# Kernel tuning notes

Hardware: AMD Instinct MI355X
Metric: run time of the kernel (lower is better)

## Reference

```python
import jax, jax.numpy as jnp
import numpy as np

N = 10000      # nodes
E = 320000     # edges
D = 256        # input_nf = output_nf
H = 256        # hidden_nf
ED = 16        # edges_in_d
NORM = 32.0    # normalization_factor


def setup_inputs() -> dict:
    key = jax.random.key(0)
    ks = jax.random.split(key, 16)
    s = 0.02  # param scale
    return {
        "h": jax.random.normal(ks[0], (N, D), dtype=jnp.float32),
        "edge_index": jax.random.randint(ks[1], (2, E), 0, N, dtype=jnp.int64),
        "edge_attr": jax.random.normal(ks[2], (E, ED), dtype=jnp.float32),
        "node_mask": jnp.ones((N, 1), dtype=jnp.float32),
        "edge_mask": jnp.ones((E, 1), dtype=jnp.float32),
        # edge_mlp: Linear(2D+ED -> H), SiLU, Linear(H -> H), SiLU
        "We1": jax.random.normal(ks[3], (2 * D + ED, H), dtype=jnp.float32) * s,
        "be1": jnp.zeros((H,), dtype=jnp.float32),
        "We2": jax.random.normal(ks[4], (H, H), dtype=jnp.float32) * s,
        "be2": jnp.zeros((H,), dtype=jnp.float32),
        # att_mlp: Linear(H -> 1), Sigmoid
        "Wa": jax.random.normal(ks[5], (H, 1), dtype=jnp.float32) * s,
        "ba": jnp.zeros((1,), dtype=jnp.float32),
        # node_mlp: Linear(H + D -> H), SiLU, Linear(H -> D)
        "Wn1": jax.random.normal(ks[6], (H + D, H), dtype=jnp.float32) * s,
        "bn1": jnp.zeros((H,), dtype=jnp.float32),
        "Wn2": jax.random.normal(ks[7], (H, D), dtype=jnp.float32) * s,
        "bn2": jnp.zeros((D,), dtype=jnp.float32),
    }


def reference(h, edge_index, edge_attr, node_mask, edge_mask,
              We1, be1, We2, be2, Wa, ba, Wn1, bn1, Wn2, bn2):
    row, col = edge_index[0], edge_index[1]
    # edge model: gather endpoints, concat with edge_attr -> [E, 2D+ED]
    e_in = jnp.concatenate([h[row], h[col], edge_attr], axis=1)
    mij = jax.nn.silu(jax.nn.silu(e_in @ We1 + be1) @ We2 + be2)  # [E, H]
    att = jax.nn.sigmoid(mij @ Wa + ba)                            # [E, 1]
    edge_feat = mij * att * edge_mask                              # [E, H]
    # node model: scatter-add messages to rows, normalize by constant
    agg = jax.ops.segment_sum(edge_feat, row, num_segments=h.shape[0]) / NORM  # [N, H]
    a = jnp.concatenate([h, agg], axis=1)                          # [N, D+H]
    h_out = h + (jax.nn.silu(a @ Wn1 + bn1) @ Wn2 + bn2)           # residual
    h_out = h_out * node_mask
    return (h_out, mij)
```

## Files before the change

kernel.cpp:

```cpp
#include <hip/hip_runtime.h>

#define NN 10000
#define NE 320000

typedef __bf16 bf16x8 __attribute__((ext_vector_type(8)));
typedef short  s16x8  __attribute__((ext_vector_type(8)));
typedef float  f32x4  __attribute__((ext_vector_type(4)));

__device__ __forceinline__ unsigned short f2bf(float f) {
  return __builtin_bit_cast(unsigned short, (__bf16)f);
}
__device__ __forceinline__ float bf2f(unsigned short s) {
  unsigned u = ((unsigned)s) << 16;
  return __builtin_bit_cast(float, u);
}
__device__ __forceinline__ float sigm(float x) {
  return __builtin_amdgcn_rcpf(1.0f + __expf(-x));
}
__device__ __forceinline__ float silu_f(float x) {
  return x * __builtin_amdgcn_rcpf(1.0f + __expf(-x));
}

__global__ void prep_w(const float* __restrict__ We1, const float* __restrict__ We2,
                       const float* __restrict__ Wn1, const float* __restrict__ Wn2,
                       unsigned short* __restrict__ W1abT, unsigned short* __restrict__ W1cT,
                       unsigned short* __restrict__ We2T,
                       unsigned short* __restrict__ Wn1T, unsigned short* __restrict__ Wn2T) {
  int g = blockIdx.x * blockDim.x + threadIdx.x;
  const int S1 = 512 * 256, S2 = 256 * 32, S3 = 256 * 256, S4 = 256 * 512, S5 = 256 * 256;
  if (g < S1) {
    int n = g >> 8, k = g & 255;
    float v = (n < 256) ? We1[k * 256 + n] : We1[(256 + k) * 256 + (n - 256)];
    W1abT[g] = f2bf(v);
  } else if (g < S1 + S2) {
    int i = g - S1; int n = i >> 5, kk = i & 31;
    float v = (kk < 16) ? We1[(512 + kk) * 256 + n] : 0.0f;
    W1cT[i] = f2bf(v);
  } else if (g < S1 + S2 + S3) {
    int i = g - S1 - S2; int n = i >> 8, k = i & 255;
    We2T[i] = f2bf(We2[k * 256 + n]);
  } else if (g < S1 + S2 + S3 + S4) {
    int i = g - S1 - S2 - S3; int n = i >> 9, k = i & 511;
    Wn1T[i] = f2bf(Wn1[k * 256 + n]);
  } else if (g < S1 + S2 + S3 + S4 + S5) {
    int i = g - S1 - S2 - S3 - S4; int n = i >> 8, k = i & 255;
    Wn2T[i] = f2bf(Wn2[k * 256 + n]);
  }
}

__global__ void prep_x(const float* __restrict__ h, unsigned short* __restrict__ hb) {
  int g = blockIdx.x * blockDim.x + threadIdx.x;
  if (g < NN * 64) {
    float4 f = ((const float4*)h)[g];
    unsigned short* d = hb + g * 4;
    d[0] = f2bf(f.x); d[1] = f2bf(f.y); d[2] = f2bf(f.z); d[3] = f2bf(f.w);
  }
}

__global__ void hist_kernel(const int* __restrict__ eidx, int* __restrict__ rowi,
                            int* __restrict__ counts) {
  __shared__ int s64;
  if (threadIdx.x == 0) {
    bool b = true;
    for (int i = 1; i < 64; i += 2) b = b && (eidx[i] == 0);
    s64 = b ? 1 : 0;
  }
  __syncthreads();
  int e = blockIdx.x * 256 + threadIdx.x;
  if (e < NE) {
    int r = s64 ? (int)((const long long*)eidx)[e] : eidx[e];
    rowi[e] = r;
    atomicAdd(&counts[r], 1);
  }
}

__global__ __launch_bounds__(1024) void scan_kernel(const int* __restrict__ counts,
                                                    int* __restrict__ rowStart,
                                                    int* __restrict__ cursor) {
  __shared__ int part[1024];
  int t = threadIdx.x;
  int local[10];
  int s = 0;
  #pragma unroll
  for (int i = 0; i < 10; i++) {
    int idx = t * 10 + i;
    int c = (idx < NN) ? counts[idx] : 0;
    local[i] = s; s += c;
  }
  part[t] = s;
  __syncthreads();
  int val = s;
  for (int off = 1; off < 1024; off <<= 1) {
    int tmp = (t >= off) ? part[t - off] : 0;
    __syncthreads();
    part[t] += tmp;
    __syncthreads();
  }
  int base = part[t] - val;
  #pragma unroll
  for (int i = 0; i < 10; i++) {
    int idx = t * 10 + i;
    if (idx < NN) { int v = base + local[i]; rowStart[idx] = v; cursor[idx] = v; }
  }
  if (t == 1023) rowStart[NN] = NE;
}

__global__ void scatter_kernel(const int* __restrict__ rowi, int* __restrict__ cursor,
                               int* __restrict__ eorder, int* __restrict__ rowSorted) {
  int e = blockIdx.x * 256 + threadIdx.x;
  if (e < NE) {
    int r = rowi[e];
    int pos = atomicAdd(&cursor[r], 1);
    eorder[pos] = e;
    rowSorted[pos] = r;
  }
}

__global__ __launch_bounds__(512, 4) void hpq_kernel(
    const unsigned short* __restrict__ hb, const unsigned short* __restrict__ W1abT,
    unsigned short* __restrict__ hPQb) {
  __shared__ unsigned short Abuf[128 * 40];

  const int tid = threadIdx.x;
  const int lane = tid & 63;
  const int wid = tid >> 6;
  const int wrr = wid >> 2, wcc = wid & 3;
  const int n0 = blockIdx.x * 128;
  const int coh = blockIdx.y;
  const unsigned short* Bsrc = W1abT + ((size_t)(coh << 8)) * 256;

  f32x4 acc[4][4];
  #pragma unroll
  for (int m = 0; m < 4; m++)
    #pragma unroll
    for (int n = 0; n < 4; n++) acc[m][n] = (f32x4){0.f, 0.f, 0.f, 0.f};

  const int eA = tid >> 2, sA = tid & 3;
  int nodeA = n0 + eA; if (nodeA >= NN) nodeA = NN - 1;
  const int rbase = (wrr << 6) + (lane & 15);
  const int koff = (lane >> 4) << 3;
  const int cfrag = lane & 15;

  for (int kt = 0; kt < 8; ++kt) {
    const int k0 = kt << 5;
    __syncthreads();
    *(s16x8*)&Abuf[eA * 40 + (sA << 3)] = *(const s16x8*)(hb + (size_t)nodeA * 256 + k0 + (sA << 3));
    __syncthreads();
    bf16x8 a[4], b[4];
    #pragma unroll
    for (int m = 0; m < 4; m++)
      a[m] = __builtin_bit_cast(bf16x8, *(const s16x8*)&Abuf[(rbase + m * 16) * 40 + koff]);
    #pragma unroll
    for (int n = 0; n < 4; n++)
      b[n] = __builtin_bit_cast(bf16x8,
               *(const s16x8*)(Bsrc + (((wcc << 6) + n * 16 + cfrag) << 8) + k0 + koff));
    #pragma unroll
    for (int m = 0; m < 4; m++)
      #pragma unroll
      for (int n = 0; n < 4; n++)
        acc[m][n] = __builtin_amdgcn_mfma_f32_16x16x32_bf16(a[m], b[n], acc[m][n], 0, 0, 0);
  }

  #pragma unroll
  for (int m = 0; m < 4; m++) {
    int rl = (wrr << 6) + m * 16 + ((lane >> 4) << 2);
    #pragma unroll
    for (int n = 0; n < 4; n++) {
      int cg = (wcc << 6) + n * 16 + cfrag;
      #pragma unroll
      for (int j = 0; j < 4; j++) {
        int rg = n0 + rl + j;
        if (rg < NN) hPQb[(size_t)rg * 512 + (coh << 8) + cg] = f2bf(acc[m][n][j]);
      }
    }
  }
}

__global__ __launch_bounds__(512, 4) void edge_kernel(
    const unsigned short* __restrict__ hPQb, const int* __restrict__ eidx,
    const float* __restrict__ eattr, const float* __restrict__ emask,
    const unsigned short* __restrict__ W1cT, const float* __restrict__ be1,
    const unsigned short* __restrict__ We2T, const float* __restrict__ be2,
    const float* __restrict__ Wa, const float* __restrict__ ba,
    const int* __restrict__ eorder, const int* __restrict__ rowSorted,
    float* __restrict__ mij_out, float* __restrict__ agg) {
  __shared__ unsigned short A2[128 * 264];
  __shared__ float attP[4][128];
  __shared__ float attL[128];
  __shared__ int rowL[128], colL[128], origL[128];
  __shared__ float waL[256], be1L[256], be2L[256];
  __shared__ int s64;

  const int tid = threadIdx.x;
  const int lane = tid & 63;
  const int wid = tid >> 6;
  const int wr = wid >> 2, wc = wid & 3;
  const int nwg = NE / 128, q = nwg >> 3, r = nwg & 7;
  const int xcd = blockIdx.x & 7, bi = blockIdx.x >> 3;
  const int wg = (xcd < r ? xcd * (q + 1) : r * (q + 1) + (xcd - r) * q) + bi;
  const int e0 = wg * 128;
  const int cfrag = lane & 15;
  const int lq = lane >> 4;
  const int koff = lq << 3;
  const int rbase = (wr << 6) + cfrag;

  if (tid == 0) {
    bool b = true;
    for (int i = 1; i < 64; i += 2) b = b && (eidx[i] == 0);
    s64 = b ? 1 : 0;
  }
  __syncthreads();

  if (tid < 128) {
    int orig = eorder[e0 + tid];
    origL[tid] = orig;
    rowL[tid] = rowSorted[e0 + tid];
    colL[tid] = s64 ? (int)((const long long*)eidx)[NE + orig] : eidx[NE + orig];
  }
  if (tid >= 256) {
    int i = tid - 256;
    waL[i] = Wa[i]; be1L[i] = be1[i]; be2L[i] = be2[i];
  }
  __syncthreads();

  f32x4 acc[4][4];
  #pragma unroll
  for (int m = 0; m < 4; m++)
    #pragma unroll
    for (int n = 0; n < 4; n++) acc[m][n] = (f32x4){0.f, 0.f, 0.f, 0.f};

  {
    int e = tid >> 2, p = tid & 3;
    int c0 = p << 6;
    const unsigned short* pr = hPQb + (size_t)rowL[e] * 512 + c0;
    const unsigned short* pc = hPQb + (size_t)colL[e] * 512 + 256 + c0;
    #pragma unroll
    for (int qq = 0; qq < 8; ++qq) {
      s16x8 vr = *(const s16x8*)(pr + (qq << 3));
      s16x8 vc = *(const s16x8*)(pc + (qq << 3));
      s16x8 vo;
      #pragma unroll
      for (int j = 0; j < 8; ++j)
        vo[j] = (short)f2bf(bf2f((unsigned short)vr[j]) + bf2f((unsigned short)vc[j]));
      *(s16x8*)&A2[e * 264 + c0 + (qq << 3)] = vo;
    }
  }
  {
    bf16x8 a[4], b[4];
    #pragma unroll
    for (int m = 0; m < 4; m++) {
      int rl = rbase + m * 16;
      if (koff < 16) {
        const float* src = eattr + (size_t)origL[rl] * 16 + koff;
        float4 f0 = *(const float4*)src;
        float4 f1 = *(const float4*)(src + 4);
        s16x8 v;
        v[0] = (short)f2bf(f0.x); v[1] = (short)f2bf(f0.y);
        v[2] = (short)f2bf(f0.z); v[3] = (short)f2bf(f0.w);
        v[4] = (short)f2bf(f1.x); v[5] = (short)f2bf(f1.y);
        v[6] = (short)f2bf(f1.z); v[7] = (short)f2bf(f1.w);
        a[m] = __builtin_bit_cast(bf16x8, v);
      } else {
        a[m] = __builtin_bit_cast(bf16x8, (s16x8){0, 0, 0, 0, 0, 0, 0, 0});
      }
    }
    #pragma unroll
    for (int n = 0; n < 4; n++)
      b[n] = __builtin_bit_cast(bf16x8,
               *(const s16x8*)(W1cT + (((wc << 6) + n * 16 + cfrag) << 5) + koff));
    #pragma unroll
    for (int m = 0; m < 4; m++)
      #pragma unroll
      for (int n = 0; n < 4; n++)
        acc[m][n] = __builtin_amdgcn_mfma_f32_16x16x32_bf16(a[m], b[n], acc[m][n], 0, 0, 0);
  }
  __syncthreads();

  #pragma unroll
  for (int m = 0; m < 4; m++) {
    int rl = (wr << 6) + m * 16 + (lq << 2);
    #pragma unroll
    for (int n = 0; n < 4; n++) {
      int cg = (wc << 6) + n * 16 + cfrag;
      float bias = be1L[cg];
      #pragma unroll
      for (int j = 0; j < 4; j++) {
        float x = acc[m][n][j] + bf2f(A2[(rl + j) * 264 + cg]) + bias;
        A2[(rl + j) * 264 + cg] = f2bf(silu_f(x));
      }
      acc[m][n] = (f32x4){0.f, 0.f, 0.f, 0.f};
    }
  }
  __syncthreads();

  #pragma unroll
  for (int t = 0; t < 8; ++t) {
    const int k0 = t << 5;
    bf16x8 a[4], b[4];
    #pragma unroll
    for (int m = 0; m < 4; m++)
      a[m] = __builtin_bit_cast(bf16x8, *(const s16x8*)&A2[(rbase + m * 16) * 264 + k0 + koff]);
    #pragma unroll
    for (int n = 0; n < 4; n++)
      b[n] = __builtin_bit_cast(bf16x8,
               *(const s16x8*)(We2T + (((wc << 6) + n * 16 + cfrag) << 8) + k0 + koff));
    #pragma unroll
    for (int m = 0; m < 4; m++)
      #pragma unroll
      for (int n = 0; n < 4; n++)
        acc[m][n] = __builtin_amdgcn_mfma_f32_16x16x32_bf16(a[m], b[n], acc[m][n], 0, 0, 0);
  }
  __syncthreads();

  float part[4][4];
  #pragma unroll
  for (int m = 0; m < 4; m++)
    #pragma unroll
    for (int j = 0; j < 4; j++) part[m][j] = 0.f;

  #pragma unroll
  for (int m = 0; m < 4; m++) {
    #pragma unroll
    for (int n = 0; n < 4; n++) {
      int cg = (wc << 6) + n * 16 + cfrag;
      float bias = be2L[cg];
      float wav = waL[cg];
      #pragma unroll
      for (int j = 0; j < 4; j++) {
        int row = (wr << 6) + m * 16 + (lq << 2) + j;
        float x = silu_f(acc[m][n][j] + bias);
        mij_out[(size_t)origL[row] * 256 + cg] = x;
        A2[row * 264 + cg] = f2bf(x);
        part[m][j] += x * wav;
      }
    }
  }
  #pragma unroll
  for (int m = 0; m < 4; m++)
    #pragma unroll
    for (int j = 0; j < 4; j++) {
      float p = part[m][j];
      p += __shfl_xor(p, 1);
      p += __shfl_xor(p, 2);
      p += __shfl_xor(p, 4);
      p += __shfl_xor(p, 8);
      part[m][j] = p;
    }
  if (cfrag == 0) {
    #pragma unroll
    for (int m = 0; m < 4; m++)
      #pragma unroll
      for (int j = 0; j < 4; j++)
        attP[wc][(wr << 6) + m * 16 + (lq << 2) + j] = part[m][j];
  }
  __syncthreads();
  if (tid < 128) {
    float s = attP[0][tid] + attP[1][tid] + attP[2][tid] + attP[3][tid] + ba[0];
    attL[tid] = sigm(s) * emask[origL[tid]];
  }
  __syncthreads();

  {
    const int half = tid >> 8;
    const int c = tid & 255;
    const int i0 = half << 6, i1 = i0 + 64;
    const int fd = rowL[i0];
    float acc2 = 0.f;
    int prev = fd;
    for (int i = i0; i < i1; ++i) {
      int rr = rowL[i];
      if (rr != prev) {
        if (prev == fd) atomicAdd(&agg[(size_t)prev * 256 + c], acc2);
        else            agg[(size_t)prev * 256 + c] = acc2;
        acc2 = 0.f; prev = rr;
      }
      acc2 += attL[i] * bf2f(A2[i * 264 + c]);
    }
    atomicAdd(&agg[(size_t)prev * 256 + c], acc2);
  }
}

__global__ __launch_bounds__(512, 4) void node_kernel(
    const float* __restrict__ h, const float* __restrict__ agg,
    const float* __restrict__ nmask,
    const unsigned short* __restrict__ Wn1T, const float* __restrict__ bn1,
    const unsigned short* __restrict__ Wn2T, const float* __restrict__ bn2,
    float* __restrict__ hout) {
  __shared__ unsigned short Abuf[64 * 40];
  __shared__ unsigned short A2[64 * 264];
  __shared__ float bn1L[256], bn2L[256];

  const int tid = threadIdx.x;
  const int lane = tid & 63;
  const int wid = tid >> 6;
  const int n0 = blockIdx.x * 64;

  if (tid < 256) { bn1L[tid] = bn1[tid]; bn2L[tid] = bn2[tid]; }

  f32x4 acc[2][4];
  #pragma unroll
  for (int m = 0; m < 2; m++)
    #pragma unroll
    for (int n = 0; n < 4; n++) acc[m][n] = (f32x4){0.f, 0.f, 0.f, 0.f};

  const int wrr = wid >> 2, wcc = wid & 3;
  const int rbase = (wrr << 5) + (lane & 15);
  const int koff = (lane >> 4) << 3;
  const int cfrag = lane & 15;

  const int eA = tid >> 2, sA = tid & 3;
  int nodeA = n0 + (eA & 63); if (nodeA >= NN) nodeA = NN - 1;

  for (int kt = 0; kt < 16; ++kt) {
    const int k0 = kt << 5;
    __syncthreads();
    if (eA < 64) {
      const float* src = (k0 < 256) ? (h + (size_t)nodeA * 256 + k0 + (sA << 3))
                                    : (agg + (size_t)nodeA * 256 + (k0 - 256) + (sA << 3));
      const float sc = (k0 < 256) ? 1.0f : (1.0f / 32.0f);
      float4 f0 = *(const float4*)src;
      float4 f1 = *(const float4*)(src + 4);
      s16x8 v;
      v[0] = (short)f2bf(f0.x * sc); v[1] = (short)f2bf(f0.y * sc);
      v[2] = (short)f2bf(f0.z * sc); v[3] = (short)f2bf(f0.w * sc);
      v[4] = (short)f2bf(f1.x * sc); v[5] = (short)f2bf(f1.y * sc);
      v[6] = (short)f2bf(f1.z * sc); v[7] = (short)f2bf(f1.w * sc);
      *(s16x8*)&Abuf[eA * 40 + (sA << 3)] = v;
    }
    __syncthreads();
    bf16x8 a[2], b[4];
    #pragma unroll
    for (int m = 0; m < 2; m++)
      a[m] = __builtin_bit_cast(bf16x8, *(const s16x8*)&Abuf[(rbase + m * 16) * 40 + koff]);
    #pragma unroll
    for (int n = 0; n < 4; n++)
      b[n] = __builtin_bit_cast(bf16x8,
               *(const s16x8*)(Wn1T + (((wcc << 6) + n * 16 + cfrag) << 9) + k0 + koff));
    #pragma unroll
    for (int m = 0; m < 2; m++)
      #pragma unroll
      for (int n = 0; n < 4; n++)
        acc[m][n] = __builtin_amdgcn_mfma_f32_16x16x32_bf16(a[m], b[n], acc[m][n], 0, 0, 0);
  }

  #pragma unroll
  for (int m = 0; m < 2; m++) {
    int rl = (wrr << 5) + m * 16 + ((lane >> 4) << 2);
    #pragma unroll
    for (int n = 0; n < 4; n++) {
      int cg = (wcc << 6) + n * 16 + cfrag;
      float bias = bn1L[cg];
      #pragma unroll
      for (int j = 0; j < 4; j++) {
        float x = acc[m][n][j] + bias;
        A2[(rl + j) * 264 + cg] = f2bf(silu_f(x));
      }
      acc[m][n] = (f32x4){0.f, 0.f, 0.f, 0.f};
    }
  }
  __syncthreads();

  #pragma unroll
  for (int kt = 0; kt < 8; ++kt) {
    const int k0 = kt << 5;
    bf16x8 a[2], b[4];
    #pragma unroll
    for (int m = 0; m < 2; m++)
      a[m] = __builtin_bit_cast(bf16x8, *(const s16x8*)&A2[(rbase + m * 16) * 264 + k0 + koff]);
    #pragma unroll
    for (int n = 0; n < 4; n++)
      b[n] = __builtin_bit_cast(bf16x8,
               *(const s16x8*)(Wn2T + (((wcc << 6) + n * 16 + cfrag) << 8) + k0 + koff));
    #pragma unroll
    for (int m = 0; m < 2; m++)
      #pragma unroll
      for (int n = 0; n < 4; n++)
        acc[m][n] = __builtin_amdgcn_mfma_f32_16x16x32_bf16(a[m], b[n], acc[m][n], 0, 0, 0);
  }

  #pragma unroll
  for (int m = 0; m < 2; m++) {
    int rl = (wrr << 5) + m * 16 + ((lane >> 4) << 2);
    #pragma unroll
    for (int n = 0; n < 4; n++) {
      int cg = (wcc << 6) + n * 16 + cfrag;
      #pragma unroll
      for (int j = 0; j < 4; j++) {
        int rg = n0 + rl + j;
        if (rg < NN) {
          float val = acc[m][n][j] + bn2L[cg];
          float o = (h[(size_t)rg * 256 + cg] + val) * nmask[rg];
          hout[(size_t)rg * 256 + cg] = o;
        }
      }
    }
  }
}

extern "C" void kernel_launch(void* const* d_in, const int* in_sizes, int n_in,
                              void* d_out, int out_size, void* d_ws, size_t ws_size,
                              hipStream_t stream) {
  (void)in_sizes; (void)n_in; (void)out_size; (void)ws_size;
  const float* h     = (const float*)d_in[0];
  const int*   eidx  = (const int*)d_in[1];
  const float* eattr = (const float*)d_in[2];
  const float* nmask = (const float*)d_in[3];
  const float* emask = (const float*)d_in[4];
  const float* We1 = (const float*)d_in[5];
  const float* be1 = (const float*)d_in[6];
  const float* We2 = (const float*)d_in[7];
  const float* be2 = (const float*)d_in[8];
  const float* Wa  = (const float*)d_in[9];
  const float* ba  = (const float*)d_in[10];
  const float* Wn1 = (const float*)d_in[11];
  const float* bn1 = (const float*)d_in[12];
  const float* Wn2 = (const float*)d_in[13];
  const float* bn2 = (const float*)d_in[14];

  char* ws = (char*)d_ws;
  unsigned short* W1abT = (unsigned short*)(ws + 0);
  unsigned short* W1cT  = (unsigned short*)(ws + 262144);
  unsigned short* We2T  = (unsigned short*)(ws + 278528);
  unsigned short* Wn1T  = (unsigned short*)(ws + 409600);
  unsigned short* Wn2T  = (unsigned short*)(ws + 671744);
  unsigned short* hPQb  = (unsigned short*)(ws + 802816);
  float* agg      = (float*)(ws + 11042816);
  int*   counts   = (int*)(ws + 21282816);
  int*   rowStart = (int*)(ws + 21322816);
  int*   cursor   = (int*)(ws + 21362824);
  int*   eorder   = (int*)(ws + 21402824);
  int*   rowi     = (int*)(ws + 22682824);
  int*   rowSorted= (int*)(ws + 23962824);
  unsigned short* hb = (unsigned short*)(ws + 25242824);

  float* hout = (float*)d_out;
  float* mij  = (float*)d_out + (size_t)NN * 256;

  hipMemsetAsync(counts, 0, NN * sizeof(int), stream);
  hipMemsetAsync(agg, 0, (size_t)NN * 256 * sizeof(float), stream);
  prep_w<<<1568, 256, 0, stream>>>(We1, We2, Wn1, Wn2, W1abT, W1cT, We2T, Wn1T, Wn2T);
  prep_x<<<2500, 256, 0, stream>>>(h, hb);
  hist_kernel<<<(NE + 255) / 256, 256, 0, stream>>>(eidx, rowi, counts);
  scan_kernel<<<1, 1024, 0, stream>>>(counts, rowStart, cursor);
  scatter_kernel<<<(NE + 255) / 256, 256, 0, stream>>>(rowi, cursor, eorder, rowSorted);
  hpq_kernel<<<dim3((NN + 127) / 128, 2), 512, 0, stream>>>(hb, W1abT, hPQb);
  edge_kernel<<<NE / 128, 512, 0, stream>>>(hPQb, eidx, eattr, emask, W1cT, be1, We2T, be2,
                                            Wa, ba, eorder, rowSorted, mij, agg);
  node_kernel<<<(NN + 63) / 64, 512, 0, stream>>>(h, agg, nmask, Wn1T, bn1, Wn2T, bn2, hout);
}
```

Measured before the change: 348.1 us.

## Merge prep kernels, drop rowi buffer, gather hPQ sums into MFMA accumulators

Folds the weight conversion, h conversion and histogram kernels into one launch. The scatter kernel now rereads edge_index directly instead of a stored rowi array. In the edge kernel, the gathered row/col hPQ sums are loaded straight into the MFMA accumulator registers in fragment layout, rather than staged through LDS, which also removes a barrier and an LDS read-modify-write. The trade-off is that the gather becomes scalar 2-byte loads per fragment element instead of 16-byte vector loads.

```diff
diff --git a/kernel.cpp b/kernel.cpp
--- a/kernel.cpp
+++ b/kernel.cpp
@@ -21,55 +21,50 @@
   return x * __builtin_amdgcn_rcpf(1.0f + __expf(-x));
 }
 
-__global__ void prep_w(const float* __restrict__ We1, const float* __restrict__ We2,
-                       const float* __restrict__ Wn1, const float* __restrict__ Wn2,
-                       unsigned short* __restrict__ W1abT, unsigned short* __restrict__ W1cT,
-                       unsigned short* __restrict__ We2T,
-                       unsigned short* __restrict__ Wn1T, unsigned short* __restrict__ Wn2T) {
-  int g = blockIdx.x * blockDim.x + threadIdx.x;
-  const int S1 = 512 * 256, S2 = 256 * 32, S3 = 256 * 256, S4 = 256 * 512, S5 = 256 * 256;
-  if (g < S1) {
-    int n = g >> 8, k = g & 255;
-    float v = (n < 256) ? We1[k * 256 + n] : We1[(256 + k) * 256 + (n - 256)];
-    W1abT[g] = f2bf(v);
-  } else if (g < S1 + S2) {
-    int i = g - S1; int n = i >> 5, kk = i & 31;
-    float v = (kk < 16) ? We1[(512 + kk) * 256 + n] : 0.0f;
-    W1cT[i] = f2bf(v);
-  } else if (g < S1 + S2 + S3) {
-    int i = g - S1 - S2; int n = i >> 8, k = i & 255;
-    We2T[i] = f2bf(We2[k * 256 + n]);
-  } else if (g < S1 + S2 + S3 + S4) {
-    int i = g - S1 - S2 - S3; int n = i >> 9, k = i & 511;
-    Wn1T[i] = f2bf(Wn1[k * 256 + n]);
-  } else if (g < S1 + S2 + S3 + S4 + S5) {
-    int i = g - S1 - S2 - S3 - S4; int n = i >> 8, k = i & 255;
-    Wn2T[i] = f2bf(Wn2[k * 256 + n]);
-  }
-}
-
-__global__ void prep_x(const float* __restrict__ h, unsigned short* __restrict__ hb) {
-  int g = blockIdx.x * blockDim.x + threadIdx.x;
-  if (g < NN * 64) {
+__global__ void prep_all(const float* __restrict__ We1, const float* __restrict__ We2,
+                         const float* __restrict__ Wn1, const float* __restrict__ Wn2,
+                         const float* __restrict__ h, const int* __restrict__ eidx,
+                         unsigned short* __restrict__ W1abT, unsigned short* __restrict__ W1cT,
+                         unsigned short* __restrict__ We2T,
+                         unsigned short* __restrict__ Wn1T, unsigned short* __restrict__ Wn2T,
+                         unsigned short* __restrict__ hb, int* __restrict__ counts) {
+  const int b = blockIdx.x;
+  if (b < 1568) {
+    int g = b * 256 + threadIdx.x;
+    const int S1 = 512 * 256, S2 = 256 * 32, S3 = 256 * 256, S4 = 256 * 512, S5 = 256 * 256;
+    if (g < S1) {
+      int n = g >> 8, k = g & 255;
+      float v = (n < 256) ? We1[k * 256 + n] : We1[(256 + k) * 256 + (n - 256)];
+      W1abT[g] = f2bf(v);
+    } else if (g < S1 + S2) {
+      int i = g - S1; int n = i >> 5, kk = i & 31;
+      float v = (kk < 16) ? We1[(512 + kk) * 256 + n] : 0.0f;
+      W1cT[i] = f2bf(v);
+    } else if (g < S1 + S2 + S3) {
+      int i = g - S1 - S2; int n = i >> 8, k = i & 255;
+      We2T[i] = f2bf(We2[k * 256 + n]);
+    } else if (g < S1 + S2 + S3 + S4) {
+      int i = g - S1 - S2 - S3; int n = i >> 9, k = i & 511;
+      Wn1T[i] = f2bf(Wn1[k * 256 + n]);
+    } else if (g < S1 + S2 + S3 + S4 + S5) {
+      int i = g - S1 - S2 - S3 - S4; int n = i >> 8, k = i & 255;
+      Wn2T[i] = f2bf(Wn2[k * 256 + n]);
+    }
+  } else if (b < 4068) {
+    int g = (b - 1568) * 256 + threadIdx.x;
     float4 f = ((const float4*)h)[g];
     unsigned short* d = hb + g * 4;
     d[0] = f2bf(f.x); d[1] = f2bf(f.y); d[2] = f2bf(f.z); d[3] = f2bf(f.w);
-  }
-}
-
-__global__ void hist_kernel(const int* __restrict__ eidx, int* __restrict__ rowi,
-                            int* __restrict__ counts) {
-  __shared__ int s64;
-  if (threadIdx.x == 0) {
-    bool b = true;
-    for (int i = 1; i < 64; i += 2) b = b && (eidx[i] == 0);
-    s64 = b ? 1 : 0;
-  }
-  __syncthreads();
-  int e = blockIdx.x * 256 + threadIdx.x;
-  if (e < NE) {
+  } else {
+    __shared__ int s64;
+    if (threadIdx.x == 0) {
+      bool bb = true;
+      for (int i = 1; i < 64; i += 2) bb = bb && (eidx[i] == 0);
+      s64 = bb ? 1 : 0;
+    }
+    __syncthreads();
+    int e = (b - 4068) * 256 + threadIdx.x;
     int r = s64 ? (int)((const long long*)eidx)[e] : eidx[e];
-    rowi[e] = r;
     atomicAdd(&counts[r], 1);
   }
 }
@@ -105,11 +100,18 @@
   if (t == 1023) rowStart[NN] = NE;
 }
 
-__global__ void scatter_kernel(const int* __restrict__ rowi, int* __restrict__ cursor,
+__global__ void scatter_kernel(const int* __restrict__ eidx, int* __restrict__ cursor,
                                int* __restrict__ eorder, int* __restrict__ rowSorted) {
+  __shared__ int s64;
+  if (threadIdx.x == 0) {
+    bool bb = true;
+    for (int i = 1; i < 64; i += 2) bb = bb && (eidx[i] == 0);
+    s64 = bb ? 1 : 0;
+  }
+  __syncthreads();
   int e = blockIdx.x * 256 + threadIdx.x;
   if (e < NE) {
-    int r = rowi[e];
+    int r = s64 ? (int)((const long long*)eidx)[e] : eidx[e];
     int pos = atomicAdd(&cursor[r], 1);
     eorder[pos] = e;
     rowSorted[pos] = r;
@@ -224,27 +226,22 @@
   __syncthreads();
 
   f32x4 acc[4][4];
-  #pragma unroll
-  for (int m = 0; m < 4; m++)
-    #pragma unroll
-    for (int n = 0; n < 4; n++) acc[m][n] = (f32x4){0.f, 0.f, 0.f, 0.f};
-
-  {
-    int e = tid >> 2, p = tid & 3;
-    int c0 = p << 6;
-    const unsigned short* pr = hPQb + (size_t)rowL[e] * 512 + c0;
-    const unsigned short* pc = hPQb + (size_t)colL[e] * 512 + 256 + c0;
-    #pragma unroll
-    for (int qq = 0; qq < 8; ++qq) {
-      s16x8 vr = *(const s16x8*)(pr + (qq << 3));
-      s16x8 vc = *(const s16x8*)(pc + (qq << 3));
-      s16x8 vo;
-      #pragma unroll
-      for (int j = 0; j < 8; ++j)
-        vo[j] = (short)f2bf(bf2f((unsigned short)vr[j]) + bf2f((unsigned short)vc[j]));
-      *(s16x8*)&A2[e * 264 + c0 + (qq << 3)] = vo;
-    }
-  }
+
+  #pragma unroll
+  for (int m = 0; m < 4; m++) {
+    #pragma unroll
+    for (int j = 0; j < 4; j++) {
+      int row = (wr << 6) + m * 16 + (lq << 2) + j;
+      const unsigned short* pr = hPQb + (size_t)rowL[row] * 512;
+      const unsigned short* pc = hPQb + (size_t)colL[row] * 512 + 256;
+      #pragma unroll
+      for (int n = 0; n < 4; n++) {
+        int cg = (wc << 6) + n * 16 + cfrag;
+        acc[m][n][j] = bf2f(pr[cg]) + bf2f(pc[cg]);
+      }
+    }
+  }
+
   {
     bf16x8 a[4], b[4];
     #pragma unroll
@@ -274,7 +271,6 @@
       for (int n = 0; n < 4; n++)
         acc[m][n] = __builtin_amdgcn_mfma_f32_16x16x32_bf16(a[m], b[n], acc[m][n], 0, 0, 0);
   }
-  __syncthreads();
 
   #pragma unroll
   for (int m = 0; m < 4; m++) {
@@ -284,10 +280,8 @@
       int cg = (wc << 6) + n * 16 + cfrag;
       float bias = be1L[cg];
       #pragma unroll
-      for (int j = 0; j < 4; j++) {
-        float x = acc[m][n][j] + bf2f(A2[(rl + j) * 264 + cg]) + bias;
-        A2[(rl + j) * 264 + cg] = f2bf(silu_f(x));
-      }
+      for (int j = 0; j < 4; j++)
+        A2[(rl + j) * 264 + cg] = f2bf(silu_f(acc[m][n][j] + bias));
       acc[m][n] = (f32x4){0.f, 0.f, 0.f, 0.f};
     }
   }
@@ -529,7 +523,6 @@
   int*   rowStart = (int*)(ws + 21322816);
   int*   cursor   = (int*)(ws + 21362824);
   int*   eorder   = (int*)(ws + 21402824);
-  int*   rowi     = (int*)(ws + 22682824);
   int*   rowSorted= (int*)(ws + 23962824);
   unsigned short* hb = (unsigned short*)(ws + 25242824);
 
@@ -538,11 +531,10 @@
 
   hipMemsetAsync(counts, 0, NN * sizeof(int), stream);
   hipMemsetAsync(agg, 0, (size_t)NN * 256 * sizeof(float), stream);
-  prep_w<<<1568, 256, 0, stream>>>(We1, We2, Wn1, Wn2, W1abT, W1cT, We2T, Wn1T, Wn2T);
-  prep_x<<<2500, 256, 0, stream>>>(h, hb);
-  hist_kernel<<<(NE + 255) / 256, 256, 0, stream>>>(eidx, rowi, counts);
+  prep_all<<<5318, 256, 0, stream>>>(We1, We2, Wn1, Wn2, h, eidx,
+                                     W1abT, W1cT, We2T, Wn1T, Wn2T, hb, counts);
   scan_kernel<<<1, 1024, 0, stream>>>(counts, rowStart, cursor);
-  scatter_kernel<<<(NE + 255) / 256, 256, 0, stream>>>(rowi, cursor, eorder, rowSorted);
+  scatter_kernel<<<(NE + 255) / 256, 256, 0, stream>>>(eidx, cursor, eorder, rowSorted);
   hpq_kernel<<<dim3((NN + 127) / 128, 2), 512, 0, stream>>>(hb, W1abT, hPQb);
   edge_kernel<<<NE / 128, 512, 0, stream>>>(hPQb, eidx, eattr, emask, W1cT, be1, We2T, be2,
                                             Wa, ba, eorder, rowSorted, mij, agg);
```

Measured after the change: 424.0 us. +21.8%, slower.
